# Optimization experiments

Hardware: AMD Instinct MI355X
Metric: run time of the kernel (lower is better)

The kernel has to match this reference:

```python
import jax, jax.numpy as jnp
import numpy as np

D_MODEL = 1024
N_HEADS = 16
D_K = D_MODEL // N_HEADS
SCALE = 1.0 / np.sqrt(D_K).astype(np.float32)
NEG = -1000000000.0


def setup_inputs() -> dict:
    key = jax.random.key(0)
    ks = jax.random.split(key, 5)
    B, S = 2, 2048
    query = jax.random.normal(ks[0], (B, S, D_MODEL), dtype=jnp.float32)
    k_in = jax.random.normal(ks[1], (B, S, D_MODEL), dtype=jnp.float32)
    v_in = jax.random.normal(ks[2], (B, S, D_MODEL), dtype=jnp.float32)
    # causal mask, broadcast over batch and heads; 0 entries get -1e9
    mask = jnp.tril(jnp.ones((S, S), dtype=jnp.int32))[None, None, :, :]
    w_qkv = jax.random.normal(ks[3], (D_MODEL, 3 * D_MODEL), dtype=jnp.float32) * (1.0 / np.sqrt(D_MODEL))
    w_o = jax.random.normal(ks[4], (D_MODEL, D_MODEL), dtype=jnp.float32) * (1.0 / np.sqrt(D_MODEL))
    return {"query": query, "key": k_in, "value": v_in, "mask": mask, "w_qkv": w_qkv, "w_o": w_o}


def reference(query, key, value, mask, w_qkv, w_o):
    # NOTE: original module ignores `key`/`value`; q,k,v all come from `query`.
    B, S, _ = query.shape
    qkv = query @ w_qkv                       # [B,S,3D]
    q, k, v = jnp.split(qkv, 3, axis=-1)
    def heads(x):
        return x.reshape(B, S, N_HEADS, D_K).transpose(0, 2, 1, 3)  # [B,H,S,dk]
    Q, K, V = heads(q), heads(k), heads(v)
    scores = jnp.einsum('bhqd,bhkd->bhqk', Q, K) * SCALE            # [B,H,S,S]
    scores = jnp.where(mask == 0, NEG, scores)
    attn = jax.nn.softmax(scores, axis=-1)
    # Dropout(0.1) treated as eval-mode identity for a deterministic reference.
    context = jnp.einsum('bhqk,bhkd->bhqd', attn, V)                # [B,H,S,dk]
    context = context.transpose(0, 2, 1, 3).reshape(B, S, D_MODEL)
    return context @ w_o
```

## Files before the change

### kernel.cpp

```cpp
#include <hip/hip_runtime.h>
#include <stdint.h>
#include <type_traits>


typedef __attribute__((ext_vector_type(8))) short bf16x8;
typedef __attribute__((ext_vector_type(4))) float f32x4;

#define LOG2E 1.44269504088896340736f
#define QSCALE (0.125f * LOG2E)

__device__ __forceinline__ unsigned short f2b(float f) {
  union { float f; unsigned int i; } x; x.f = f;
  unsigned int i = x.i;
  return (unsigned short)((i + 0x7FFFu + ((i >> 16) & 1u)) >> 16);
}
__device__ __forceinline__ unsigned short f2b_trunc(float f) {
  union { float f; unsigned int i; } x; x.f = f;
  return (unsigned short)(x.i >> 16);
}

__device__ __forceinline__ void async16(const void* g, void* l) {
  __builtin_amdgcn_global_load_lds(
      (__attribute__((address_space(1))) void*)g,
      (__attribute__((address_space(3))) void*)l, 16, 0, 0);
}

__device__ __forceinline__ f32x4 mfma16(bf16x8 a, bf16x8 b, f32x4 c) {
  return __builtin_amdgcn_mfma_f32_16x16x32_bf16(a, b, c, 0, 0, 0);
}

__global__ __launch_bounds__(256) void cvt_x(const float* __restrict__ src,
                                             unsigned short* __restrict__ dst) {
  const size_t i = ((size_t)blockIdx.x * 256 + threadIdx.x) * 8;
  float4 a = *(const float4*)(src + i);
  float4 b = *(const float4*)(src + i + 4);
  unsigned short e[8];
  e[0] = f2b(a.x); e[1] = f2b(a.y); e[2] = f2b(a.z); e[3] = f2b(a.w);
  e[4] = f2b(b.x); e[5] = f2b(b.y); e[6] = f2b(b.z); e[7] = f2b(b.w);
  *(uint4*)(dst + i) = *(const uint4*)e;
}

__global__ __launch_bounds__(256) void transpose_cvt(
    const float* __restrict__ src, unsigned short* __restrict__ dst, int R,
    int Ccols, int scale_cols, float scale) {
  __shared__ __align__(16) unsigned short Lt[64 * 64];
  const int r0 = blockIdx.x * 64, c0 = blockIdx.y * 64;
  const float s = (c0 < scale_cols) ? scale : 1.0f;
  const int t = threadIdx.x;
#pragma unroll
  for (int it = 0; it < 4; ++it) {
    int c = it * 256 + t;
    int sr = c >> 4, co = (c & 15) * 4;
    float4 v = *(const float4*)(src + (size_t)(r0 + sr) * Ccols + c0 + co);
    Lt[(co + 0) * 64 + sr] = f2b(v.x * s);
    Lt[(co + 1) * 64 + sr] = f2b(v.y * s);
    Lt[(co + 2) * 64 + sr] = f2b(v.z * s);
    Lt[(co + 3) * 64 + sr] = f2b(v.w * s);
  }
  __syncthreads();
#pragma unroll
  for (int it = 0; it < 2; ++it) {
    int c = it * 256 + t;
    int dr = c >> 3, so = (c & 7) * 8;
    *(uint4*)(dst + (size_t)(c0 + dr) * R + r0 + so) =
        *(const uint4*)(Lt + dr * 64 + so);
  }
}

template <typename CT>
__global__ __launch_bounds__(256) void gemm_bt(
    const unsigned short* __restrict__ A, const unsigned short* __restrict__ Bt,
    CT* __restrict__ C, int M, int N, int K) {
  __shared__ __align__(16) unsigned short As[128 * 32];
  __shared__ __align__(16) unsigned short Bs[128 * 32];
  const int t = threadIdx.x;
  const int w = t >> 6, l = t & 63;
  const int m0 = blockIdx.y * 128, n0 = blockIdx.x * 128;
  const int wm = (w >> 1) * 64, wn = (w & 1) * 64;
  const int lrow = l & 15, lk = (l >> 4) * 8;

  f32x4 acc[4][4] = {};

  for (int k0 = 0; k0 < K; k0 += 32) {
    __syncthreads();
#pragma unroll
    for (int r = 0; r < 2; ++r) {
      const int c = r * 256 + t;
      async16(A + (size_t)(m0 + (c >> 2)) * K + k0 + (c & 3) * 8,
              As + (size_t)(r * 256 + w * 64) * 8);
      async16(Bt + (size_t)(n0 + (c >> 2)) * K + k0 + (c & 3) * 8,
              Bs + (size_t)(r * 256 + w * 64) * 8);
    }
    asm volatile("s_waitcnt vmcnt(0)" ::: "memory");
    __syncthreads();

    bf16x8 af[4], bf[4];
#pragma unroll
    for (int i = 0; i < 4; ++i)
      af[i] = *(const bf16x8*)(As + (wm + i * 16 + lrow) * 32 + lk);
#pragma unroll
    for (int j = 0; j < 4; ++j)
      bf[j] = *(const bf16x8*)(Bs + (wn + j * 16 + lrow) * 32 + lk);
#pragma unroll
    for (int i = 0; i < 4; ++i)
#pragma unroll
      for (int j = 0; j < 4; ++j)
        acc[i][j] = mfma16(af[i], bf[j], acc[i][j]);
  }

#pragma unroll
  for (int i = 0; i < 4; ++i)
#pragma unroll
    for (int j = 0; j < 4; ++j)
#pragma unroll
      for (int r = 0; r < 4; ++r) {
        int gr = m0 + wm + i * 16 + (l >> 4) * 4 + r;
        int gc = n0 + wn + j * 16 + (l & 15);
        if constexpr (std::is_same<CT, unsigned short>::value)
          C[(size_t)gr * N + gc] = f2b(acc[i][j][r]);
        else
          C[(size_t)gr * N + gc] = acc[i][j][r];
      }
}

__global__ __launch_bounds__(256) void gemm_o(
    const unsigned short* __restrict__ A, const unsigned short* __restrict__ Bt,
    float* __restrict__ C, int M, int N, int K) {
  __shared__ __align__(16) unsigned short As[64 * 32];
  __shared__ __align__(16) unsigned short Bs[128 * 32];
  const int t = threadIdx.x;
  const int w = t >> 6, l = t & 63;
  const int m0 = blockIdx.y * 64, n0 = blockIdx.x * 128;
  const int wm = (w & 1) * 32, wn = (w >> 1) * 64;
  const int lrow = l & 15, lk = (l >> 4) * 8;

  f32x4 acc[2][4] = {};

  for (int k0 = 0; k0 < K; k0 += 32) {
    __syncthreads();
    async16(A + (size_t)(m0 + (t >> 2)) * K + k0 + (t & 3) * 8,
            As + (size_t)(w * 64) * 8);
#pragma unroll
    for (int r = 0; r < 2; ++r) {
      const int c = r * 256 + t;
      async16(Bt + (size_t)(n0 + (c >> 2)) * K + k0 + (c & 3) * 8,
              Bs + (size_t)(r * 256 + w * 64) * 8);
    }
    asm volatile("s_waitcnt vmcnt(0)" ::: "memory");
    __syncthreads();

    bf16x8 af[2], bf[4];
#pragma unroll
    for (int i = 0; i < 2; ++i)
      af[i] = *(const bf16x8*)(As + (wm + i * 16 + lrow) * 32 + lk);
#pragma unroll
    for (int j = 0; j < 4; ++j)
      bf[j] = *(const bf16x8*)(Bs + (wn + j * 16 + lrow) * 32 + lk);
#pragma unroll
    for (int i = 0; i < 2; ++i)
#pragma unroll
      for (int j = 0; j < 4; ++j)
        acc[i][j] = mfma16(af[i], bf[j], acc[i][j]);
  }

#pragma unroll
  for (int i = 0; i < 2; ++i)
#pragma unroll
    for (int j = 0; j < 4; ++j)
#pragma unroll
      for (int r = 0; r < 4; ++r) {
        int gr = m0 + wm + i * 16 + (l >> 4) * 4 + r;
        int gc = n0 + wn + j * 16 + (l & 15);
        C[(size_t)gr * N + gc] = acc[i][j][r];
      }
}

__global__ __launch_bounds__(256) void v_relayout(
    const unsigned short* __restrict__ qkv, unsigned short* __restrict__ Vt) {
  __shared__ __align__(16) unsigned short Lt[64 * 64];
  const int s0 = blockIdx.x * 64;
  const int bh = blockIdx.y;
  const int b = bh >> 4, h = bh & 15;
  const int t = threadIdx.x;
#pragma unroll
  for (int r = 0; r < 2; ++r) {
    int c = r * 256 + t;
    int sr = c >> 3, doff = (c & 7) * 8;
    uint4 v = *(const uint4*)(qkv + (size_t)(b * 2048 + s0 + sr) * 3072 + 2048 +
                              h * 64 + doff);
    const unsigned short* e = (const unsigned short*)&v;
#pragma unroll
    for (int j = 0; j < 8; ++j) Lt[(doff + j) * 64 + sr] = e[j];
  }
  __syncthreads();
#pragma unroll
  for (int r = 0; r < 2; ++r) {
    int c = r * 256 + t;
    int dr = c >> 3, so = (c & 7) * 8;
    *(uint4*)(Vt + ((size_t)bh * 64 + dr) * 2048 + s0 + so) =
        *(const uint4*)(Lt + dr * 64 + so);
  }
}

__global__ __launch_bounds__(512) void attn_fwd(
    const unsigned short* __restrict__ qkv,
    const unsigned short* __restrict__ Vt,
    unsigned short* __restrict__ ctx) {
  __shared__ __align__(16) unsigned short Ks[2][64 * 64];
  __shared__ __align__(16) unsigned short Vs[2][64 * 64];
  __shared__ __align__(16) unsigned short Ps[8][16 * 72];

  const int ti = blockIdx.x;
  const int bh = blockIdx.y;
  const int b = bh >> 4, h = bh & 15;
  const int t = threadIdx.x;
  const int g = t >> 8;
  const int tl = t & 255;
  const int w = tl >> 6;
  const int gw = t >> 6;
  const int l = t & 63;
  const int lm = l & 15, lq = l >> 4;
  const int sw = lm & 7;
  const int c0 = (lq ^ sw) * 8;
  const int c1 = ((lq + 4) ^ sw) * 8;

  const int qt0[2] = {ti * 64, (31 - ti) * 64};
  const int ktmax = 31 - ti;
  const int nsup = (ktmax >> 1) + 1;

  const unsigned short* Qp = qkv + (size_t)(b * 2048) * 3072 + h * 64;
  const unsigned short* Kp = qkv + (size_t)(b * 2048) * 3072 + 1024 + h * 64;
  const unsigned short* Vb = Vt + (size_t)bh * 64 * 2048;

  bf16x8 qf[2][2];
#pragma unroll
  for (int qt = 0; qt < 2; ++qt) {
    const int qrow = qt0[qt] + w * 16 + lm;
    qf[qt][0] = *(const bf16x8*)(Qp + (size_t)qrow * 3072 + lq * 8);
    qf[qt][1] = *(const bf16x8*)(Qp + (size_t)qrow * 3072 + 32 + lq * 8);
  }

  f32x4 oacc[2][4] = {};
  float lsum[2][4] = {{0.f, 0.f, 0.f, 0.f}, {0.f, 0.f, 0.f, 0.f}};

  for (int jj = 0; jj < nsup; ++jj) {
    const int kt = 2 * jj + g;
    const bool have = (kt <= ktmax);
    __syncthreads();
    if (have) {
      const int kk0 = kt * 64;
#pragma unroll
      for (int r = 0; r < 2; ++r) {
        int cl = r * 256 + tl;
        int row = cl >> 3, cp = cl & 7;
        int so = ((cp ^ (row & 7)) * 8);
        async16(Kp + (size_t)(kk0 + row) * 3072 + so,
                Ks[g] + (size_t)(r * 256 + w * 64) * 8);
        async16(Vb + (size_t)row * 2048 + kk0 + so,
                Vs[g] + (size_t)(r * 256 + w * 64) * 8);
      }
    }
    asm volatile("s_waitcnt vmcnt(0)" ::: "memory");
    __syncthreads();
    if (!have) continue;

    const unsigned short* Kc = Ks[g];
    const unsigned short* Vc = Vs[g];

#pragma unroll
    for (int qt = 0; qt < 2; ++qt) {
      if (qt == 0 && kt > ti) continue;
      f32x4 sacc[4] = {};
#pragma unroll
      for (int nt = 0; nt < 4; ++nt) {
        const unsigned short* kr = Kc + (nt * 16 + lm) * 64;
        bf16x8 bk0 = *(const bf16x8*)(kr + c0);
        bf16x8 bk1 = *(const bf16x8*)(kr + c1);
        sacc[nt] = mfma16(qf[qt][0], bk0, sacc[nt]);
        sacc[nt] = mfma16(qf[qt][1], bk1, sacc[nt]);
      }

      const bool diag = (kt == ((qt == 0) ? ti : ktmax));
#pragma unroll
      for (int nt = 0; nt < 4; ++nt)
#pragma unroll
        for (int r = 0; r < 4; ++r) {
          float p = exp2f(sacc[nt][r]);
          if (diag && (nt * 16 + lm) > (w * 16 + lq * 4 + r)) p = 0.f;
          lsum[qt][r] += p;
          Ps[gw][(lq * 4 + r) * 72 + nt * 16 + lm] = f2b_trunc(p);
        }
      asm volatile("s_waitcnt lgkmcnt(0)" ::: "memory");

#pragma unroll
      for (int ks = 0; ks < 2; ++ks) {
        bf16x8 pa = *(const bf16x8*)(&Ps[gw][lm * 72 + ks * 32 + lq * 8]);
        const int cc = (ks == 0) ? c0 : c1;
#pragma unroll
        for (int nt = 0; nt < 4; ++nt) {
          bf16x8 vb = *(const bf16x8*)(Vc + (nt * 16 + lm) * 64 + cc);
          oacc[qt][nt] = mfma16(pa, vb, oacc[qt][nt]);
        }
      }
    }
  }

#pragma unroll
  for (int qt = 0; qt < 2; ++qt)
#pragma unroll
    for (int d = 1; d < 16; d <<= 1)
#pragma unroll
      for (int r = 0; r < 4; ++r)
        lsum[qt][r] += __shfl_xor(lsum[qt][r], d, 64);

  __syncthreads();
  float* fbuf[2] = {(float*)Ks, (float*)Vs};
  float* lbuf = (float*)Ps;
  if (g == 1) {
#pragma unroll
    for (int qt = 0; qt < 2; ++qt) {
#pragma unroll
      for (int nt = 0; nt < 4; ++nt)
#pragma unroll
        for (int r = 0; r < 4; ++r)
          fbuf[qt][(w * 16 + lq * 4 + r) * 64 + nt * 16 + lm] = oacc[qt][nt][r];
      if (lm == 0)
#pragma unroll
        for (int r = 0; r < 4; ++r)
          lbuf[qt * 64 + w * 16 + lq * 4 + r] = lsum[qt][r];
    }
  }
  __syncthreads();
  if (g == 0) {
#pragma unroll
    for (int qt = 0; qt < 2; ++qt) {
      float rinv[4];
#pragma unroll
      for (int r = 0; r < 4; ++r)
        rinv[r] = 1.f / (lsum[qt][r] + lbuf[qt * 64 + w * 16 + lq * 4 + r]);
#pragma unroll
      for (int nt = 0; nt < 4; ++nt)
#pragma unroll
        for (int r = 0; r < 4; ++r) {
          float v = oacc[qt][nt][r] +
                    fbuf[qt][(w * 16 + lq * 4 + r) * 64 + nt * 16 + lm];
          size_t tok = (size_t)b * 2048 + qt0[qt] + w * 16 + lq * 4 + r;
          ctx[tok * 1024 + h * 64 + nt * 16 + lm] = f2b(v * rinv[r]);
        }
    }
  }
}

extern "C" void kernel_launch(void* const* d_in, const int* in_sizes, int n_in,
                              void* d_out, int out_size, void* d_ws,
                              size_t ws_size, hipStream_t stream) {
  const float* query = (const float*)d_in[0];
  const float* w_qkv = (const float*)d_in[4];
  const float* w_o = (const float*)d_in[5];
  float* out = (float*)d_out;

  unsigned short* ws = (unsigned short*)d_ws;
  unsigned short* wqkvT = ws;
  unsigned short* woT = wqkvT + (size_t)3072 * 1024;
  unsigned short* Xb = woT + (size_t)1024 * 1024;
  unsigned short* qkv = Xb + (size_t)4096 * 1024;
  unsigned short* Vt = qkv + (size_t)4096 * 3072;
  unsigned short* ctx = Xb;

  cvt_x<<<dim3(2048), 256, 0, stream>>>(query, Xb);
  transpose_cvt<<<dim3(16, 48), 256, 0, stream>>>(w_qkv, wqkvT, 1024, 3072,
                                                  1024, QSCALE);
  transpose_cvt<<<dim3(16, 16), 256, 0, stream>>>(w_o, woT, 1024, 1024, 0,
                                                  1.0f);
  gemm_bt<unsigned short><<<dim3(24, 32), 256, 0, stream>>>(Xb, wqkvT, qkv,
                                                            4096, 3072, 1024);
  v_relayout<<<dim3(32, 32), 256, 0, stream>>>(qkv, Vt);
  attn_fwd<<<dim3(16, 32), 512, 0, stream>>>(qkv, Vt, ctx);
  gemm_o<<<dim3(8, 64), 256, 0, stream>>>(ctx, woT, out, 4096, 1024, 1024);
}
```

Baseline: 221.7 us.

## Compute transposed S tile so each lane owns one query row in attention

Swaps the MFMA operands for QK^T so the score tile comes out transposed and each lane holds four consecutive keys for a single query row. This lets the kernel pack four bf16 probabilities into one 8-byte LDS store instead of four scalar stores, and keep one row sum per lane, which needs fewer cross-lane shuffles. V fragments are now loaded from LDS once per key tile and reused for both query tiles. It also switches to the raw hardware exp2 builtin and adds a min-occupancy hint to launch_bounds, which may raise register pressure or cause spills.

```diff
diff --git a/kernel.cpp b/kernel.cpp
--- a/kernel.cpp
+++ b/kernel.cpp
@@ -14,10 +14,6 @@
   unsigned int i = x.i;
   return (unsigned short)((i + 0x7FFFu + ((i >> 16) & 1u)) >> 16);
 }
-__device__ __forceinline__ unsigned short f2b_trunc(float f) {
-  union { float f; unsigned int i; } x; x.f = f;
-  return (unsigned short)(x.i >> 16);
-}
 
 __device__ __forceinline__ void async16(const void* g, void* l) {
   __builtin_amdgcn_global_load_lds(
@@ -27,6 +23,11 @@
 
 __device__ __forceinline__ f32x4 mfma16(bf16x8 a, bf16x8 b, f32x4 c) {
   return __builtin_amdgcn_mfma_f32_16x16x32_bf16(a, b, c, 0, 0, 0);
+}
+
+__device__ __forceinline__ unsigned int fbits(float f) {
+  union { float f; unsigned int i; } x; x.f = f;
+  return x.i;
 }
 
 __global__ __launch_bounds__(256) void cvt_x(const float* __restrict__ src,
@@ -202,7 +203,7 @@
   }
 }
 
-__global__ __launch_bounds__(512) void attn_fwd(
+__global__ __launch_bounds__(512, 4) void attn_fwd(
     const unsigned short* __restrict__ qkv,
     const unsigned short* __restrict__ Vt,
     unsigned short* __restrict__ ctx) {
@@ -241,7 +242,7 @@
   }
 
   f32x4 oacc[2][4] = {};
-  float lsum[2][4] = {{0.f, 0.f, 0.f, 0.f}, {0.f, 0.f, 0.f, 0.f}};
+  float lsum[2] = {0.f, 0.f};
 
   for (int jj = 0; jj < nsup; ++jj) {
     const int kt = 2 * jj + g;
@@ -267,51 +268,65 @@
     const unsigned short* Kc = Ks[g];
     const unsigned short* Vc = Vs[g];
 
+    bf16x8 vf[8];
+#pragma unroll
+    for (int nt = 0; nt < 4; ++nt) {
+      const unsigned short* vr = Vc + (nt * 16 + lm) * 64;
+      vf[nt] = *(const bf16x8*)(vr + c0);
+      vf[4 + nt] = *(const bf16x8*)(vr + c1);
+    }
+
 #pragma unroll
     for (int qt = 0; qt < 2; ++qt) {
       if (qt == 0 && kt > ti) continue;
       f32x4 sacc[4] = {};
 #pragma unroll
-      for (int nt = 0; nt < 4; ++nt) {
-        const unsigned short* kr = Kc + (nt * 16 + lm) * 64;
+      for (int mt = 0; mt < 4; ++mt) {
+        const unsigned short* kr = Kc + (mt * 16 + lm) * 64;
         bf16x8 bk0 = *(const bf16x8*)(kr + c0);
         bf16x8 bk1 = *(const bf16x8*)(kr + c1);
-        sacc[nt] = mfma16(qf[qt][0], bk0, sacc[nt]);
-        sacc[nt] = mfma16(qf[qt][1], bk1, sacc[nt]);
+        sacc[mt] = mfma16(bk0, qf[qt][0], sacc[mt]);
+        sacc[mt] = mfma16(bk1, qf[qt][1], sacc[mt]);
       }
 
       const bool diag = (kt == ((qt == 0) ? ti : ktmax));
-#pragma unroll
-      for (int nt = 0; nt < 4; ++nt)
-#pragma unroll
-        for (int r = 0; r < 4; ++r) {
-          float p = exp2f(sacc[nt][r]);
-          if (diag && (nt * 16 + lm) > (w * 16 + lq * 4 + r)) p = 0.f;
-          lsum[qt][r] += p;
-          Ps[gw][(lq * 4 + r) * 72 + nt * 16 + lm] = f2b_trunc(p);
+      const int qloc = w * 16 + lm;
+#pragma unroll
+      for (int mt = 0; mt < 4; ++mt) {
+        float p0 = __builtin_amdgcn_exp2f(sacc[mt][0]);
+        float p1 = __builtin_amdgcn_exp2f(sacc[mt][1]);
+        float p2 = __builtin_amdgcn_exp2f(sacc[mt][2]);
+        float p3 = __builtin_amdgcn_exp2f(sacc[mt][3]);
+        if (diag) {
+          const int kvb = mt * 16 + lq * 4;
+          if (kvb + 0 > qloc) p0 = 0.f;
+          if (kvb + 1 > qloc) p1 = 0.f;
+          if (kvb + 2 > qloc) p2 = 0.f;
+          if (kvb + 3 > qloc) p3 = 0.f;
         }
+        lsum[qt] += (p0 + p1) + (p2 + p3);
+        uint2 pk;
+        pk.x = (fbits(p1) & 0xFFFF0000u) | (fbits(p0) >> 16);
+        pk.y = (fbits(p3) & 0xFFFF0000u) | (fbits(p2) >> 16);
+        *(uint2*)(&Ps[gw][lm * 72 + mt * 16 + lq * 4]) = pk;
+      }
       asm volatile("s_waitcnt lgkmcnt(0)" ::: "memory");
 
 #pragma unroll
       for (int ks = 0; ks < 2; ++ks) {
         bf16x8 pa = *(const bf16x8*)(&Ps[gw][lm * 72 + ks * 32 + lq * 8]);
-        const int cc = (ks == 0) ? c0 : c1;
-#pragma unroll
-        for (int nt = 0; nt < 4; ++nt) {
-          bf16x8 vb = *(const bf16x8*)(Vc + (nt * 16 + lm) * 64 + cc);
-          oacc[qt][nt] = mfma16(pa, vb, oacc[qt][nt]);
-        }
-      }
-    }
-  }
-
-#pragma unroll
-  for (int qt = 0; qt < 2; ++qt)
-#pragma unroll
-    for (int d = 1; d < 16; d <<= 1)
-#pragma unroll
-      for (int r = 0; r < 4; ++r)
-        lsum[qt][r] += __shfl_xor(lsum[qt][r], d, 64);
+#pragma unroll
+        for (int nt = 0; nt < 4; ++nt)
+          oacc[qt][nt] = mfma16(pa, vf[ks * 4 + nt], oacc[qt][nt]);
+      }
+    }
+  }
+
+#pragma unroll
+  for (int qt = 0; qt < 2; ++qt) {
+    lsum[qt] += __shfl_xor(lsum[qt], 16, 64);
+    lsum[qt] += __shfl_xor(lsum[qt], 32, 64);
+  }
 
   __syncthreads();
   float* fbuf[2] = {(float*)Ks, (float*)Vs};
@@ -324,20 +339,18 @@
 #pragma unroll
         for (int r = 0; r < 4; ++r)
           fbuf[qt][(w * 16 + lq * 4 + r) * 64 + nt * 16 + lm] = oacc[qt][nt][r];
-      if (lm == 0)
-#pragma unroll
-        for (int r = 0; r < 4; ++r)
-          lbuf[qt * 64 + w * 16 + lq * 4 + r] = lsum[qt][r];
+      if (l < 16) lbuf[qt * 64 + w * 16 + lm] = lsum[qt];
     }
   }
   __syncthreads();
   if (g == 0) {
 #pragma unroll
     for (int qt = 0; qt < 2; ++qt) {
+      const float ltot = lsum[qt] + lbuf[qt * 64 + w * 16 + lm];
       float rinv[4];
 #pragma unroll
       for (int r = 0; r < 4; ++r)
-        rinv[r] = 1.f / (lsum[qt][r] + lbuf[qt * 64 + w * 16 + lq * 4 + r]);
+        rinv[r] = 1.f / __shfl(ltot, lq * 4 + r, 64);
 #pragma unroll
       for (int nt = 0; nt < 4; ++nt)
 #pragma unroll
```

After: 218.0 us. About the same (-1.6%).
